# Kernel optimization log

Hardware: AMD Instinct MI355X
Metric: run time of the kernel (lower is better)

The kernel has to match this reference:

```python
import jax, jax.numpy as jnp
import numpy as np

T, B, D = 2048, 32, 1024


def setup_inputs() -> dict:
    key = jax.random.key(0)
    k1, k2, k3 = jax.random.split(key, 3)
    x = jax.random.normal(k1, (T, B, D), dtype=jnp.float32)
    h0 = jnp.zeros((B, D), dtype=jnp.float32)
    # xavier-uniform-ish init: std ~= sqrt(2/(fan_in+fan_out)) = sqrt(1/D); W_h uses gain 0.5
    std = (1.0 / D) ** 0.5
    W_x = jax.random.normal(k2, (D, D), dtype=jnp.float32) * std
    W_h = jax.random.normal(k3, (D, D), dtype=jnp.float32) * (0.5 * std)
    b = jnp.zeros((D,), dtype=jnp.float32)
    return {"x": x, "h0": h0, "W_x": W_x, "W_h": W_h, "b": b}


def reference(x, h0, W_x, W_h, b):
    # h_t = tanh(x_t @ W_x + h_{t-1} @ W_h + b)   (haste stock-elman layout)
    # Precompute the input projection for all timesteps in one big GEMM.
    xW = jnp.einsum('tbd,de->tbe', x, W_x) + b  # [T, B, D]

    def step(h_prev, xw_t):
        h_new = jnp.tanh(xw_t + h_prev @ W_h)
        return h_new, h_new

    _, hs = jax.lax.scan(step, h0, xW)  # hs: [T, B, D]
    h_all = jnp.concatenate([h0[None], hs], axis=0)  # [T+1, B, D]
    return hs, h_all
```

## Files before the change

kernel.cpp:

```cpp
#include <hip/hip_runtime.h>
#include <hip/hip_fp16.h>

#define T_STEPS 2048
#define BATCH   32
#define DIM     1024
#define NWG     32
#define WCOLS   32

typedef _Float16 half2_t __attribute__((ext_vector_type(2)));
typedef _Float16 f16x8 __attribute__((ext_vector_type(8)));
typedef float    f32x4 __attribute__((ext_vector_type(4)));

__device__ __forceinline__ f16x8 cvt8(f32x4 a, f32x4 b) {
    f16x8 r;
    r[0]=(_Float16)a[0]; r[1]=(_Float16)a[1]; r[2]=(_Float16)a[2]; r[3]=(_Float16)a[3];
    r[4]=(_Float16)b[0]; r[5]=(_Float16)b[1]; r[6]=(_Float16)b[2]; r[7]=(_Float16)b[3];
    return r;
}

__global__ void flag_init(int* __restrict__ flags) { flags[threadIdx.x] = 0; }

__global__ void conv_pack(const float* __restrict__ Wh, _Float16* __restrict__ P) {
    const int idx = blockIdx.x * blockDim.x + threadIdx.x;
    const int k = idx >> 10, n = idx & (DIM - 1);
    const int pos = (k >> 3) ^ (n & 7);
    P[(size_t)n * 1024 + pos * 8 + (k & 7)] = (_Float16)Wh[idx];
}

#define BM 128
#define BN 128
#define BK 32
#define LDT 40

__global__ __launch_bounds__(256) void gemm_xw(
    const float* __restrict__ X, const float* __restrict__ Wx,
    const float* __restrict__ bias, float* __restrict__ out)
{
    __shared__ _Float16 As[BM][LDT];
    __shared__ _Float16 Bs[BN][LDT];

    const int tid = threadIdx.x;
    const int m0 = blockIdx.x * BM, n0 = blockIdx.y * BN;
    const int lane = tid & 63, wid = tid >> 6;
    const int wm = (wid >> 1) * 64, wn = (wid & 1) * 64;
    const int lr = lane & 15, lk = (lane >> 4) * 8;
    const int ar = tid >> 1, ac = (tid & 1) * 16;
    const int bk = tid >> 3, bn = (tid & 7) * 16;

    f32x4 acc[4][4] = {};

    for (int k0 = 0; k0 < DIM; k0 += BK) {
        __syncthreads();
        {
            const float* src = X + (size_t)(m0 + ar) * DIM + k0 + ac;
            float4 q0 = *(const float4*)(src + 0);
            float4 q1 = *(const float4*)(src + 4);
            float4 q2 = *(const float4*)(src + 8);
            float4 q3 = *(const float4*)(src + 12);
            f16x8 p0, p1;
            p0[0]=(_Float16)q0.x; p0[1]=(_Float16)q0.y; p0[2]=(_Float16)q0.z; p0[3]=(_Float16)q0.w;
            p0[4]=(_Float16)q1.x; p0[5]=(_Float16)q1.y; p0[6]=(_Float16)q1.z; p0[7]=(_Float16)q1.w;
            p1[0]=(_Float16)q2.x; p1[1]=(_Float16)q2.y; p1[2]=(_Float16)q2.z; p1[3]=(_Float16)q2.w;
            p1[4]=(_Float16)q3.x; p1[5]=(_Float16)q3.y; p1[6]=(_Float16)q3.z; p1[7]=(_Float16)q3.w;
            *(f16x8*)&As[ar][ac] = p0;
            *(f16x8*)&As[ar][ac + 8] = p1;
        }
        {
            const float* src = Wx + (size_t)(k0 + bk) * DIM + n0 + bn;
            float4 q0 = *(const float4*)(src + 0);
            float4 q1 = *(const float4*)(src + 4);
            float4 q2 = *(const float4*)(src + 8);
            float4 q3 = *(const float4*)(src + 12);
            float vv[16];
            *(float4*)&vv[0] = q0; *(float4*)&vv[4] = q1;
            *(float4*)&vv[8] = q2; *(float4*)&vv[12] = q3;
            #pragma unroll
            for (int i = 0; i < 16; ++i) Bs[bn + i][bk] = (_Float16)vv[i];
        }
        __syncthreads();
        f16x8 a[4], bb[4];
        #pragma unroll
        for (int f = 0; f < 4; ++f) a[f]  = *(const f16x8*)&As[wm + f * 16 + lr][lk];
        #pragma unroll
        for (int f = 0; f < 4; ++f) bb[f] = *(const f16x8*)&Bs[wn + f * 16 + lr][lk];
        #pragma unroll
        for (int i = 0; i < 4; ++i)
            #pragma unroll
            for (int j = 0; j < 4; ++j)
                acc[i][j] = __builtin_amdgcn_mfma_f32_16x16x32_f16(a[i], bb[j], acc[i][j], 0, 0, 0);
    }

    #pragma unroll
    for (int i = 0; i < 4; ++i)
        #pragma unroll
        for (int j = 0; j < 4; ++j) {
            const int col = n0 + wn + j * 16 + lr;
            const float bv = bias[col];
            #pragma unroll
            for (int r = 0; r < 4; ++r) {
                const int row = m0 + wm + i * 16 + (lane >> 4) * 4 + r;
                __builtin_nontemporal_store(acc[i][j][r] + bv, out + (size_t)row * DIM + col);
            }
        }
}

__global__ __launch_bounds__(256, 1) void elman_rec(
    const float* __restrict__ h0, const _Float16* __restrict__ P,
    float* __restrict__ hs, float* __restrict__ h_all,
    int* __restrict__ flags, _Float16* __restrict__ xchg)
{
    __shared__ _Float16 Hs[32 * 128 * 8];
    __shared__ _Float16 Ws[32 * 128 * 8];
    __shared__ float    Ht2[4][32][36];

    const int wg  = blockIdx.x;
    const int tid = threadIdx.x;
    const int w = tid >> 6, lane = tid & 63, lr = lane & 15, kg = lane >> 4;
    const int wcol0 = wg * WCOLS;

    {
        const uint4* src = (const uint4*)(P + (size_t)wcol0 * 1024);
        uint4* dst = (uint4*)Ws;
        #pragma unroll
        for (int j = 0; j < 16; ++j) dst[tid + 256 * j] = src[tid + 256 * j];
    }
    #pragma unroll
    for (int j = 0; j < 16; ++j) {
        const int bi = tid + 256 * j;
        const int r = bi >> 7, blk = bi & 127;
        f32x4 q0 = *(const f32x4*)(h0 + (size_t)r * DIM + blk * 8);
        f32x4 q1 = *(const f32x4*)(h0 + (size_t)r * DIM + blk * 8 + 4);
        *(f16x8*)&Hs[((r << 7) + (blk ^ (r & 7))) * 8] = cvt8(q0, q1);
        if (wg == 0) {
            *(f32x4*)(h_all + (size_t)r * DIM + blk * 8)     = q0;
            *(f32x4*)(h_all + (size_t)r * DIM + blk * 8 + 4) = q1;
        }
    }
    __syncthreads();

    const int er = tid >> 3, ec4 = (tid & 7) * 4;
    const int rl_rh  = lane >> 5;
    const int rl_blk = 32 * w + (lane & 31);

    for (int t = 0; t < T_STEPS; ++t) {
        float* slot = h_all + (size_t)(t + 1) * (BATCH * DIM);

        f32x4 xw = *(const f32x4*)(slot + (size_t)er * DIM + wcol0 + ec4);

        f32x4 a00 = {0,0,0,0}, a01 = {0,0,0,0}, a10 = {0,0,0,0}, a11 = {0,0,0,0};
        #pragma unroll
        for (int q = 0; q < 8; ++q) {
            const int blk = (w * 8 + q) * 4 + kg;
            const int pa = blk ^ (lr & 7);
            f16x8 A0 = *(const f16x8*)&Hs[((lr << 7)        + pa) * 8];
            f16x8 A1 = *(const f16x8*)&Hs[(((16 + lr) << 7) + pa) * 8];
            f16x8 B0 = *(const f16x8*)&Ws[((lr << 7)        + pa) * 8];
            f16x8 B1 = *(const f16x8*)&Ws[(((16 + lr) << 7) + pa) * 8];
            a00 = __builtin_amdgcn_mfma_f32_16x16x32_f16(A0, B0, a00, 0, 0, 0);
            a01 = __builtin_amdgcn_mfma_f32_16x16x32_f16(A0, B1, a01, 0, 0, 0);
            a10 = __builtin_amdgcn_mfma_f32_16x16x32_f16(A1, B0, a10, 0, 0, 0);
            a11 = __builtin_amdgcn_mfma_f32_16x16x32_f16(A1, B1, a11, 0, 0, 0);
        }
        #pragma unroll
        for (int r = 0; r < 4; ++r) {
            Ht2[w][kg * 4 + r]      [lr]      = a00[r];
            Ht2[w][kg * 4 + r]      [16 + lr] = a01[r];
            Ht2[w][16 + kg * 4 + r] [lr]      = a10[r];
            Ht2[w][16 + kg * 4 + r] [16 + lr] = a11[r];
        }
        __syncthreads();

        f32x4 z = xw;
        #pragma unroll
        for (int ww = 0; ww < 4; ++ww) z += *(const f32x4*)&Ht2[ww][er][ec4];
        f32x4 h;
        #pragma unroll
        for (int i = 0; i < 4; ++i) {
            const float e = __expf(2.0f * z[i]);
            h[i] = 1.0f - 2.0f / (e + 1.0f);
        }
        {
            half2_t lo, hi;
            lo[0] = (_Float16)h[0]; lo[1] = (_Float16)h[1];
            hi[0] = (_Float16)h[2]; hi[1] = (_Float16)h[3];
            uint2 pk;
            pk.x = __builtin_bit_cast(unsigned, lo);
            pk.y = __builtin_bit_cast(unsigned, hi);
            _Float16* xp = xchg + (size_t)((t + 1) & 1) * (BATCH * DIM)
                         + (size_t)er * DIM + wcol0 + ec4;
            asm volatile("global_store_dwordx2 %0, %1, off sc1"
                         :: "v"(xp), "v"(pk) : "memory");
        }
        __builtin_nontemporal_store(h, (f32x4*)(hs + (size_t)t * (BATCH * DIM)
                                                + (size_t)er * DIM + wcol0 + ec4));
        *(f32x4*)(slot + (size_t)er * DIM + wcol0 + ec4) = h;

        if (t == T_STEPS - 1) break;

        asm volatile("s_waitcnt vmcnt(0)" ::: "memory");
        __syncthreads();
        if (tid == 0)
            __hip_atomic_store(flags + wg * 16, t + 1, __ATOMIC_RELAXED,
                               __HIP_MEMORY_SCOPE_AGENT);

        if (lane < 8) {
            const int* fp = flags + (w * 8 + lane) * 16;
            int g = 0;
            while (__hip_atomic_load(fp, __ATOMIC_RELAXED,
                                     __HIP_MEMORY_SCOPE_AGENT) < t + 1) {
                if (++g > (1 << 20)) break;
            }
        }

        const _Float16* xb = xchg + (size_t)((t + 1) & 1) * (BATCH * DIM);
        uint4 q[16];
        #pragma unroll
        for (int i = 0; i < 16; ++i) {
            const int row = 2 * i + rl_rh;
            const _Float16* ap = xb + (size_t)row * DIM + rl_blk * 8;
            asm volatile("global_load_dwordx4 %0, %1, off sc1"
                         : "=v"(q[i]) : "v"(ap) : "memory");
        }
        asm volatile("s_waitcnt vmcnt(0)" ::: "memory");
        __builtin_amdgcn_sched_barrier(0);
        #pragma unroll
        for (int i = 0; i < 16; ++i) {
            const int row = 2 * i + rl_rh;
            *(uint4*)&Hs[((row << 7) + (rl_blk ^ (row & 7))) * 8] = q[i];
        }
    }
}

extern "C" void kernel_launch(void* const* d_in, const int* in_sizes, int n_in,
                              void* d_out, int out_size, void* d_ws, size_t ws_size,
                              hipStream_t stream) {
    const float* x    = (const float*)d_in[0];
    const float* h0   = (const float*)d_in[1];
    const float* Wx   = (const float*)d_in[2];
    const float* Wh   = (const float*)d_in[3];
    const float* bias = (const float*)d_in[4];

    float* hs    = (float*)d_out;
    float* h_all = hs + (size_t)T_STEPS * BATCH * DIM;

    int*       flags = (int*)d_ws;
    _Float16*  xchg  = (_Float16*)((char*)d_ws + 4096);
    _Float16*  P     = (_Float16*)((char*)d_ws + 4096 + 131072);

    flag_init<<<1, NWG * 16, 0, stream>>>(flags);
    conv_pack<<<(DIM * DIM) / 256, 256, 0, stream>>>(Wh, P);

    dim3 g((T_STEPS * BATCH) / BM, DIM / BN);
    gemm_xw<<<g, 256, 0, stream>>>(x, Wx, bias, h_all + (size_t)BATCH * DIM);

    elman_rec<<<NWG, 256, 0, stream>>>(h0, P, hs, h_all, flags, xchg);
}
```

Measured before the change: 7.424 ms.

## Use per-wave flags, double-buffered fp16 partials, and defer fp32 output stores

Replaces the workgroup barrier plus single per-WG flag with per-wavefront flags that each wave publishes and polls directly, removing one __syncthreads from the critical path of each step. Cross-wave partial sums are stored as fp16 in a double-buffered LDS array, so the next step's writes don't race with the previous read without a barrier. The fp32 hs/h_all stores are moved after the exchange read so they leave the inter-WG critical path. The fp16 partial sums reduce accuracy, and there are more flags to poll.

Result: slower. 8.367 ms (+12.7%).

```diff
diff --git a/kernel.cpp b/kernel.cpp
--- a/kernel.cpp
+++ b/kernel.cpp
@@ -8,6 +8,7 @@
 #define WCOLS   32
 
 typedef _Float16 half2_t __attribute__((ext_vector_type(2)));
+typedef _Float16 f16x4 __attribute__((ext_vector_type(4)));
 typedef _Float16 f16x8 __attribute__((ext_vector_type(8)));
 typedef float    f32x4 __attribute__((ext_vector_type(4)));
 
@@ -18,7 +19,7 @@
     return r;
 }
 
-__global__ void flag_init(int* __restrict__ flags) { flags[threadIdx.x] = 0; }
+__global__ void flag_init(int* __restrict__ f) { f[threadIdx.x] = 0; }
 
 __global__ void conv_pack(const float* __restrict__ Wh, _Float16* __restrict__ P) {
     const int idx = blockIdx.x * blockDim.x + threadIdx.x;
@@ -111,7 +112,7 @@
 {
     __shared__ _Float16 Hs[32 * 128 * 8];
     __shared__ _Float16 Ws[32 * 128 * 8];
-    __shared__ float    Ht2[4][32][36];
+    __shared__ _Float16 ht2h[2 * 4 * 32 * 36];
 
     const int wg  = blockIdx.x;
     const int tid = threadIdx.x;
@@ -139,12 +140,11 @@
     __syncthreads();
 
     const int er = tid >> 3, ec4 = (tid & 7) * 4;
-    const int rl_rh  = lane >> 5;
+    const int rl_rh = lane >> 5;
     const int rl_blk = 32 * w + (lane & 31);
 
     for (int t = 0; t < T_STEPS; ++t) {
         float* slot = h_all + (size_t)(t + 1) * (BATCH * DIM);
-
         f32x4 xw = *(const f32x4*)(slot + (size_t)er * DIM + wcol0 + ec4);
 
         f32x4 a00 = {0,0,0,0}, a01 = {0,0,0,0}, a10 = {0,0,0,0}, a11 = {0,0,0,0};
@@ -152,33 +152,51 @@
         for (int q = 0; q < 8; ++q) {
             const int blk = (w * 8 + q) * 4 + kg;
             const int pa = blk ^ (lr & 7);
-            f16x8 A0 = *(const f16x8*)&Hs[((lr << 7)        + pa) * 8];
+            f16x8 A0 = *(const f16x8*)&Hs[((lr << 7) + pa) * 8];
             f16x8 A1 = *(const f16x8*)&Hs[(((16 + lr) << 7) + pa) * 8];
-            f16x8 B0 = *(const f16x8*)&Ws[((lr << 7)        + pa) * 8];
+            f16x8 B0 = *(const f16x8*)&Ws[((lr << 7) + pa) * 8];
             f16x8 B1 = *(const f16x8*)&Ws[(((16 + lr) << 7) + pa) * 8];
             a00 = __builtin_amdgcn_mfma_f32_16x16x32_f16(A0, B0, a00, 0, 0, 0);
             a01 = __builtin_amdgcn_mfma_f32_16x16x32_f16(A0, B1, a01, 0, 0, 0);
             a10 = __builtin_amdgcn_mfma_f32_16x16x32_f16(A1, B0, a10, 0, 0, 0);
             a11 = __builtin_amdgcn_mfma_f32_16x16x32_f16(A1, B1, a11, 0, 0, 0);
         }
-        #pragma unroll
-        for (int r = 0; r < 4; ++r) {
-            Ht2[w][kg * 4 + r]      [lr]      = a00[r];
-            Ht2[w][kg * 4 + r]      [16 + lr] = a01[r];
-            Ht2[w][16 + kg * 4 + r] [lr]      = a10[r];
-            Ht2[w][16 + kg * 4 + r] [16 + lr] = a11[r];
+        {
+            _Float16* hb = ht2h + (size_t)(t & 1) * (4 * 32 * 36) + (size_t)w * (32 * 36);
+            #pragma unroll
+            for (int r = 0; r < 4; ++r) {
+                hb[(kg * 4 + r) * 36 + lr]           = (_Float16)a00[r];
+                hb[(kg * 4 + r) * 36 + 16 + lr]      = (_Float16)a01[r];
+                hb[(16 + kg * 4 + r) * 36 + lr]      = (_Float16)a10[r];
+                hb[(16 + kg * 4 + r) * 36 + 16 + lr] = (_Float16)a11[r];
+            }
         }
         __syncthreads();
 
         f32x4 z = xw;
-        #pragma unroll
-        for (int ww = 0; ww < 4; ++ww) z += *(const f32x4*)&Ht2[ww][er][ec4];
+        {
+            const _Float16* hb = ht2h + (size_t)(t & 1) * (4 * 32 * 36);
+            #pragma unroll
+            for (int ww = 0; ww < 4; ++ww) {
+                f16x4 pv = *(const f16x4*)&hb[(ww * 32 + er) * 36 + ec4];
+                z[0] += (float)pv[0]; z[1] += (float)pv[1];
+                z[2] += (float)pv[2]; z[3] += (float)pv[3];
+            }
+        }
         f32x4 h;
         #pragma unroll
         for (int i = 0; i < 4; ++i) {
             const float e = __expf(2.0f * z[i]);
             h[i] = 1.0f - 2.0f / (e + 1.0f);
         }
+
+        if (t == T_STEPS - 1) {
+            __builtin_nontemporal_store(h, (f32x4*)(hs + (size_t)t * (BATCH * DIM)
+                                                    + (size_t)er * DIM + wcol0 + ec4));
+            *(f32x4*)(slot + (size_t)er * DIM + wcol0 + ec4) = h;
+            break;
+        }
+
         {
             half2_t lo, hi;
             lo[0] = (_Float16)h[0]; lo[1] = (_Float16)h[1];
@@ -191,25 +209,17 @@
             asm volatile("global_store_dwordx2 %0, %1, off sc1"
                          :: "v"(xp), "v"(pk) : "memory");
         }
-        __builtin_nontemporal_store(h, (f32x4*)(hs + (size_t)t * (BATCH * DIM)
-                                                + (size_t)er * DIM + wcol0 + ec4));
-        *(f32x4*)(slot + (size_t)er * DIM + wcol0 + ec4) = h;
-
-        if (t == T_STEPS - 1) break;
-
         asm volatile("s_waitcnt vmcnt(0)" ::: "memory");
-        __syncthreads();
-        if (tid == 0)
-            __hip_atomic_store(flags + wg * 16, t + 1, __ATOMIC_RELAXED,
-                               __HIP_MEMORY_SCOPE_AGENT);
-
-        if (lane < 8) {
-            const int* fp = flags + (w * 8 + lane) * 16;
-            int g = 0;
-            while (__hip_atomic_load(fp, __ATOMIC_RELAXED,
-                                     __HIP_MEMORY_SCOPE_AGENT) < t + 1) {
-                if (++g > (1 << 20)) break;
-            }
+        if (lane == 0)
+            __hip_atomic_store(flags + (wg * 4 + w) * 4, t + 1,
+                               __ATOMIC_RELAXED, __HIP_MEMORY_SCOPE_AGENT);
+
+        if (lane < 32) {
+            const int* fp = flags + ((8 * w + (lane >> 2)) * 4 + (lane & 3)) * 4;
+            int g = 0, v;
+            do {
+                v = __hip_atomic_load(fp, __ATOMIC_RELAXED, __HIP_MEMORY_SCOPE_AGENT);
+            } while (v < t + 1 && ++g < (1 << 20));
         }
 
         const _Float16* xb = xchg + (size_t)((t + 1) & 1) * (BATCH * DIM);
@@ -228,6 +238,10 @@
             const int row = 2 * i + rl_rh;
             *(uint4*)&Hs[((row << 7) + (rl_blk ^ (row & 7))) * 8] = q[i];
         }
+
+        __builtin_nontemporal_store(h, (f32x4*)(hs + (size_t)t * (BATCH * DIM)
+                                                + (size_t)er * DIM + wcol0 + ec4));
+        *(f32x4*)(slot + (size_t)er * DIM + wcol0 + ec4) = h;
     }
 }
 
@@ -247,7 +261,7 @@
     _Float16*  xchg  = (_Float16*)((char*)d_ws + 4096);
     _Float16*  P     = (_Float16*)((char*)d_ws + 4096 + 131072);
 
-    flag_init<<<1, NWG * 16, 0, stream>>>(flags);
+    flag_init<<<1, 1024, 0, stream>>>((int*)d_ws);
     conv_pack<<<(DIM * DIM) / 256, 256, 0, stream>>>(Wh, P);
 
     dim3 g((T_STEPS * BATCH) / BM, DIM / BN);
```
